# Kernel tuning notes

Hardware: AMD Instinct MI355X
Metric: run time of the kernel (lower is better)

The kernel has to match this reference:

```python
import jax, jax.numpy as jnp
import numpy as np

B, T, TREF, NBINS, H = 4096, 8192, 8192, 50, 32  # np.linspace(lo,hi,50) -> 49 bins
EPS = 1e-10


def setup_inputs() -> dict:
    key = jax.random.key(0)
    k0, k1, k2, k3, k4, k5 = jax.random.split(key, 6)
    return {
        "current_returns": jax.random.normal(k0, (B, T), jnp.float32) * 0.02,
        "reference_returns": jax.random.normal(k1, (TREF,), jnp.float32) * 0.02,
        "w1": jax.random.normal(k2, (H, 1), jnp.float32) * 0.5,   # Linear(1, H).weight
        "b1": jax.random.normal(k3, (H,), jnp.float32) * 0.1,
        "w2": jax.random.normal(k4, (H, H), jnp.float32) * 0.1,   # Linear(H, H).weight
        "b2": jax.random.normal(k5, (H,), jnp.float32) * 0.1,
    }


def _kl_from_hists(ref, curr, ref_min, ref_max):
    # Faithful to InformationTheory.kl_divergence with n_bins=50 (49 equal-width bins).
    nb = NBINS - 1
    lo = jnp.minimum(ref_min, curr.min())
    hi = jnp.maximum(ref_max, curr.max())
    width = (hi - lo) / nb

    def hist_density(x):
        # np.histogram(x, bins=linspace(lo,hi,50), density=True); all x in [lo,hi],
        # right edge goes to last bin (handled by clip).
        idx = jnp.clip(jnp.floor((x - lo) / width).astype(jnp.int32), 0, nb - 1)
        counts = jnp.zeros(nb, jnp.float32).at[idx].add(1.0)
        return counts / (x.shape[0] * width)

    p = hist_density(ref) + EPS
    q = hist_density(curr) + EPS
    p = p / p.sum()
    q = q / q.sum()
    return jnp.sum(p * jnp.log(p / q))


def reference(current_returns, reference_returns, w1, b1, w2, b2):
    ref = reference_returns
    ref_min, ref_max = ref.min(), ref.max()
    kl = jax.vmap(lambda c: _kl_from_hists(ref, c, ref_min, ref_max))(current_returns)  # [B]
    kl = jax.lax.stop_gradient(kl)  # original detaches before building kl_tensor
    x = kl[:, None]                                  # [B, 1]
    h = jax.nn.relu(x @ w1.T + b1)                   # [B, H]
    encoded = h @ w2.T + b2                          # [B, H]
    return kl, encoded
```

## Files before the change

kernel.cpp:

```cpp
#include <hip/hip_runtime.h>
#include <math.h>

constexpr int T_LEN  = 8192;
constexpr int B_ROWS = 4096;
constexpr int NB     = 49;
constexpr int NC     = 32;
constexpr int HDIM   = 32;
constexpr int FBINS  = 8192;
constexpr int RPB    = 8;
constexpr int RECW   = 52;
constexpr float EPSF = 1e-10f;

constexpr int WS_CDF_OFF    = 8;
constexpr int WS_BINNED_OFF = 8208;

#define HP(i) ((i) + ((i) >> 5))

__device__ __forceinline__ void sync_lds() {
    asm volatile("s_waitcnt lgkmcnt(0)" ::: "memory");
    __builtin_amdgcn_s_barrier();
    __builtin_amdgcn_sched_barrier(0);
}

__global__ __launch_bounds__(256)
void ref_cdf_kernel(const float* __restrict__ ref, float* __restrict__ wsf) {
    __shared__ float sv[FBINS];
    __shared__ int   hist[HP(FBINS)];
    __shared__ int   wsum[4];
    __shared__ float rmn4[4], rmx4[4];
    const int tid  = threadIdx.x;
    const int lane = tid & 63;
    const int wave = tid >> 6;

    const float4* r4 = (const float4*)ref;
    float4* sv4 = (float4*)sv;
    float mn = 3.0e38f, mx = -3.0e38f;
    #pragma unroll
    for (int i = 0; i < 8; ++i) {
        float4 v = r4[tid + i * 256];
        sv4[tid + i * 256] = v;
        mn = fminf(mn, fminf(fminf(v.x, v.y), fminf(v.z, v.w)));
        mx = fmaxf(mx, fmaxf(fmaxf(v.x, v.y), fmaxf(v.z, v.w)));
    }
    for (int i = tid; i < HP(FBINS); i += 256) hist[i] = 0;
    #pragma unroll
    for (int off = 32; off > 0; off >>= 1) {
        mn = fminf(mn, __shfl_xor(mn, off));
        mx = fmaxf(mx, __shfl_xor(mx, off));
    }
    if (lane == 0) { rmn4[wave] = mn; rmx4[wave] = mx; }
    __syncthreads();
    const float rmin = fminf(fminf(rmn4[0], rmn4[1]), fminf(rmn4[2], rmn4[3]));
    const float rmax = fmaxf(fmaxf(rmx4[0], rmx4[1]), fmaxf(rmx4[2], rmx4[3]));
    const float finv = (float)FBINS / (rmax - rmin);

    for (int i = tid; i < FBINS; i += 256) {
        int fb = min(max((int)((sv[i] - rmin) * finv), 0), FBINS - 1);
        atomicAdd(&hist[HP(fb)], 1);
    }
    __syncthreads();

    const int base = tid * 32;
    int s = 0;
    #pragma unroll
    for (int j = 0; j < 32; ++j) {
        int h = hist[HP(base + j)]; hist[HP(base + j)] = s; s += h;
    }
    const int own = s;
    int incl = s;
    #pragma unroll
    for (int off = 1; off < 64; off <<= 1) {
        int t = __shfl_up(incl, off);
        if (lane >= off) incl += t;
    }
    if (lane == 63) wsum[wave] = incl;
    __syncthreads();
    int woff = 0;
    #pragma unroll
    for (int w = 0; w < 4; ++w) if (w < wave) woff += wsum[w];
    const int add = woff + incl - own;
    #pragma unroll
    for (int j = 0; j < 32; ++j) hist[HP(base + j)] += add;
    __syncthreads();

    int* cdf = (int*)(wsf + WS_CDF_OFF);
    for (int i = tid; i < FBINS; i += 256) cdf[i] = hist[HP(i)];
    if (tid == 0) { cdf[FBINS] = T_LEN; wsf[0] = rmin; wsf[1] = rmax; }
    __syncthreads();

    float* binned = wsf + WS_BINNED_OFF;
    for (int i = tid; i < FBINS; i += 256) {
        float x = sv[i];
        int fb = min(max((int)((x - rmin) * finv), 0), FBINS - 1);
        int pos = atomicAdd(&hist[HP(fb)], 1);
        binned[pos] = x;
    }
}

__global__ __launch_bounds__(256, 2)
void kl_pipe_kernel(const float* __restrict__ cur,
                    const float* __restrict__ wsf,
                    const float* __restrict__ w1,
                    const float* __restrict__ b1,
                    const float* __restrict__ w2,
                    const float* __restrict__ b2,
                    float* __restrict__ kl_out,
                    float* __restrict__ enc_out) {
    __shared__ float    buf[2][T_LEN];
    __shared__ unsigned hq[NC * NB];
    __shared__ float    scmn[4], scmx[4];
    __shared__ float    rec[RPB][RECW];

    const int tid  = threadIdx.x;
    const int lane = tid & 63;
    const int wave = tid >> 6;
    const int rbase = blockIdx.x * RPB;
    const float* src = cur + (size_t)rbase * T_LEN;
    const float rmin = wsf[0], rmax = wsf[1];

    auto stage = [&](int r, int pbuf) {
        const float* g = src + (size_t)r * T_LEN + wave * 2048;
        #pragma unroll
        for (int i = 0; i < 8; ++i) {
            __builtin_amdgcn_global_load_lds(
                (const __attribute__((address_space(1))) void*)(g + i * 256 + lane * 4),
                (__attribute__((address_space(3))) void*)&buf[pbuf][wave * 2048 + i * 256],
                16, 0, 0);
        }
    };

    stage(0, 0);

    #pragma unroll
    for (int r = 0; r < RPB; ++r) {
        if (r + 1 < RPB) stage(r + 1, (r + 1) & 1);

        for (int i = tid; i < NC * NB; i += 256) hq[i] = 0u;

        if (r + 1 < RPB) {
            asm volatile("s_waitcnt vmcnt(8)" ::: "memory");
        } else {
            asm volatile("s_waitcnt vmcnt(0)" ::: "memory");
        }
        __builtin_amdgcn_sched_barrier(0);

        const float4* b4 = (const float4*)buf[r & 1];
        float4 v[8];
        #pragma unroll
        for (int i = 0; i < 8; ++i) v[i] = b4[wave * 512 + i * 64 + lane];

        float mn = 3.0e38f, mx = -3.0e38f;
        #pragma unroll
        for (int i = 0; i < 8; ++i) {
            mn = fminf(mn, fminf(fminf(v[i].x, v[i].y), fminf(v[i].z, v[i].w)));
            mx = fmaxf(mx, fmaxf(fmaxf(v[i].x, v[i].y), fmaxf(v[i].z, v[i].w)));
        }
        #pragma unroll
        for (int off = 32; off > 0; off >>= 1) {
            mn = fminf(mn, __shfl_xor(mn, off));
            mx = fmaxf(mx, __shfl_xor(mx, off));
        }
        if (lane == 0) { scmn[wave] = mn; scmx[wave] = mx; }
        sync_lds();

        const float lo = fminf(rmin,
            fminf(fminf(scmn[0], scmn[1]), fminf(scmn[2], scmn[3])));
        const float hi = fmaxf(rmax,
            fmaxf(fmaxf(scmx[0], scmx[1]), fmaxf(scmx[2], scmx[3])));
        const float width = (hi - lo) / (float)NB;
        const float winv = 1.0f / width, nlw = -lo * winv;

        unsigned* myq = hq + (tid & (NC - 1)) * NB;
        #pragma unroll
        for (int i = 0; i < 8; ++i) {
            int i0 = min((int)fmaf(v[i].x, winv, nlw), NB - 1);
            int i1 = min((int)fmaf(v[i].y, winv, nlw), NB - 1);
            int i2 = min((int)fmaf(v[i].z, winv, nlw), NB - 1);
            int i3 = min((int)fmaf(v[i].w, winv, nlw), NB - 1);
            atomicAdd(&myq[i0], 1u); atomicAdd(&myq[i1], 1u);
            atomicAdd(&myq[i2], 1u); atomicAdd(&myq[i3], 1u);
        }
        sync_lds();

        if (tid < NB) {
            unsigned sq = 0u;
            #pragma unroll
            for (int c = 0; c < NC; ++c) sq += hq[c * NB + tid];
            rec[r][tid] = (float)sq;
        }
        if (tid == NB)     rec[r][NB]     = lo;
        if (tid == NB + 1) rec[r][NB + 1] = width;
        sync_lds();
    }

    for (int rr = wave; rr < RPB; rr += 4) {
        const float lo = rec[rr][NB], width = rec[rr][NB + 1];
        const bool act = lane < NB;
        const float inv = 1.0f / ((float)T_LEN * width);
        float p = 0.0f, q = 0.0f;
        if (act) q = rec[rr][lane] * inv + EPSF;

        int C = T_LEN;
        if (lane < NB - 1) {
            const float kp1  = (float)(lane + 1);
            const float finv = (float)FBINS / (rmax - rmin);
            const int* cdf = (const int*)(wsf + WS_CDF_OFF);
            const float* binned = wsf + WS_BINNED_OFF;
            const float t = fmaf(width, kp1, lo);
            int fb = (int)floorf((t - rmin) * finv);
            int a  = min(max(fb - 2, 0), FBINS);
            int bb = min(max(fb + 3, 0), FBINS);
            int ia = cdf[a], ib = cdf[bb];
            C = ia;
            for (int i = ia; i < ib; i += 4) {
                float x0 = binned[i];
                float x1 = (i + 1 < ib) ? binned[i + 1] : 3.0e38f;
                float x2 = (i + 2 < ib) ? binned[i + 2] : 3.0e38f;
                float x3 = (i + 3 < ib) ? binned[i + 3] : 3.0e38f;
                C += ((x0 - lo) / width < kp1) ? 1 : 0;
                C += ((x1 - lo) / width < kp1) ? 1 : 0;
                C += ((x2 - lo) / width < kp1) ? 1 : 0;
                C += ((x3 - lo) / width < kp1) ? 1 : 0;
            }
        }
        int Cprev = __shfl_up(C, 1);
        if (lane == 0) Cprev = 0;
        if (act) p = (float)(C - Cprev) * inv + EPSF;

        float P = p, Q = q;
        #pragma unroll
        for (int off = 32; off > 0; off >>= 1) {
            P += __shfl_xor(P, off);
            Q += __shfl_xor(Q, off);
        }
        float term = 0.0f;
        if (act) {
            const float pn = p / P;
            const float qn = q / Q;
            term = pn * logf(pn / qn);
        }
        #pragma unroll
        for (int off = 32; off > 0; off >>= 1) term += __shfl_xor(term, off);
        if (lane == 0) kl_out[rbase + rr] = term;

        if (lane < HDIM) {
            float acc = b2[lane];
            #pragma unroll
            for (int t2 = 0; t2 < HDIM; ++t2) {
                float h = fmaxf(fmaf(term, w1[t2], b1[t2]), 0.0f);
                acc = fmaf(h, w2[lane * HDIM + t2], acc);
            }
            enc_out[(size_t)(rbase + rr) * HDIM + lane] = acc;
        }
    }
}

extern "C" void kernel_launch(void* const* d_in, const int* in_sizes, int n_in,
                              void* d_out, int out_size, void* d_ws, size_t ws_size,
                              hipStream_t stream) {
    const float* cur = (const float*)d_in[0];
    const float* ref = (const float*)d_in[1];
    const float* w1  = (const float*)d_in[2];
    const float* b1  = (const float*)d_in[3];
    const float* w2  = (const float*)d_in[4];
    const float* b2  = (const float*)d_in[5];
    float* out = (float*)d_out;
    float* wsf = (float*)d_ws;

    ref_cdf_kernel<<<1, 256, 0, stream>>>(ref, wsf);
    kl_pipe_kernel<<<B_ROWS / RPB, 256, 0, stream>>>(
        cur, wsf, w1, b1, w2, b2, out, out + B_ROWS);
}
```

Baseline: 49.98 us.

## Deepen row prefetch into a chunked LDS ring two rows ahead

Replaces the double-buffered whole-row staging with an 8-slot ring of 2048-float chunks, and keeps two rows of asynchronous global-to-LDS loads in flight. Min/max scanning now waits per chunk with graded vmcnt values, so compute can start before the whole row has arrived. Loads for row r+2 are issued inside the histogram loop of row r, right after each chunk slot has been read back into registers, which overlaps memory traffic with the LDS atomics. Values are read from LDS twice (once for min/max, once for binning) instead of being held in registers, and correctness depends on the vmcnt counts matching exactly.

```diff
diff --git a/kernel.cpp b/kernel.cpp
--- a/kernel.cpp
+++ b/kernel.cpp
@@ -8,6 +8,7 @@
 constexpr int HDIM   = 32;
 constexpr int FBINS  = 8192;
 constexpr int RPB    = 8;
+constexpr int CHUNK  = 2048;
 constexpr int RECW   = 52;
 constexpr float EPSF = 1e-10f;
 
@@ -15,6 +16,9 @@
 constexpr int WS_BINNED_OFF = 8208;
 
 #define HP(i) ((i) + ((i) >> 5))
+
+#define WAITV(N) do { asm volatile("s_waitcnt vmcnt(" #N ")" ::: "memory"); \
+                      __builtin_amdgcn_sched_barrier(0); } while (0)
 
 __device__ __forceinline__ void sync_lds() {
     asm volatile("s_waitcnt lgkmcnt(0)" ::: "memory");
@@ -98,7 +102,7 @@
 }
 
 __global__ __launch_bounds__(256, 2)
-void kl_pipe_kernel(const float* __restrict__ cur,
+void kl_deep_kernel(const float* __restrict__ cur,
                     const float* __restrict__ wsf,
                     const float* __restrict__ w1,
                     const float* __restrict__ b1,
@@ -106,7 +110,7 @@
                     const float* __restrict__ b2,
                     float* __restrict__ kl_out,
                     float* __restrict__ enc_out) {
-    __shared__ float    buf[2][T_LEN];
+    __shared__ float    ring[8][CHUNK];
     __shared__ unsigned hq[NC * NB];
     __shared__ float    scmn[4], scmx[4];
     __shared__ float    rec[RPB][RECW];
@@ -118,43 +122,26 @@
     const float* src = cur + (size_t)rbase * T_LEN;
     const float rmin = wsf[0], rmax = wsf[1];
 
-    auto stage = [&](int r, int pbuf) {
-        const float* g = src + (size_t)r * T_LEN + wave * 2048;
-        #pragma unroll
-        for (int i = 0; i < 8; ++i) {
+    auto issue_chunk = [&](int r, int c) {
+        const int slot = ((r & 1) << 2) | c;
+        const float* g = src + (size_t)r * T_LEN + c * CHUNK + wave * 512 + lane * 4;
+        #pragma unroll
+        for (int i = 0; i < 2; ++i) {
             __builtin_amdgcn_global_load_lds(
-                (const __attribute__((address_space(1))) void*)(g + i * 256 + lane * 4),
-                (__attribute__((address_space(3))) void*)&buf[pbuf][wave * 2048 + i * 256],
+                (const __attribute__((address_space(1))) void*)(g + i * 256),
+                (__attribute__((address_space(3))) void*)&ring[slot][wave * 512 + i * 256],
                 16, 0, 0);
         }
     };
-
-    stage(0, 0);
-
-    #pragma unroll
-    for (int r = 0; r < RPB; ++r) {
-        if (r + 1 < RPB) stage(r + 1, (r + 1) & 1);
-
-        for (int i = tid; i < NC * NB; i += 256) hq[i] = 0u;
-
-        if (r + 1 < RPB) {
-            asm volatile("s_waitcnt vmcnt(8)" ::: "memory");
-        } else {
-            asm volatile("s_waitcnt vmcnt(0)" ::: "memory");
-        }
-        __builtin_amdgcn_sched_barrier(0);
-
-        const float4* b4 = (const float4*)buf[r & 1];
-        float4 v[8];
-        #pragma unroll
-        for (int i = 0; i < 8; ++i) v[i] = b4[wave * 512 + i * 64 + lane];
-
-        float mn = 3.0e38f, mx = -3.0e38f;
-        #pragma unroll
-        for (int i = 0; i < 8; ++i) {
-            mn = fminf(mn, fminf(fminf(v[i].x, v[i].y), fminf(v[i].z, v[i].w)));
-            mx = fmaxf(mx, fmaxf(fmaxf(v[i].x, v[i].y), fmaxf(v[i].z, v[i].w)));
-        }
+    auto mmchunk = [&](int slot, float& mn, float& mx) {
+        const float4* q = (const float4*)&ring[slot][wave * 512];
+        float4 a0 = q[lane], a1 = q[lane + 64];
+        mn = fminf(mn, fminf(fminf(a0.x, a0.y), fminf(a0.z, a0.w)));
+        mx = fmaxf(mx, fmaxf(fmaxf(a0.x, a0.y), fmaxf(a0.z, a0.w)));
+        mn = fminf(mn, fminf(fminf(a1.x, a1.y), fminf(a1.z, a1.w)));
+        mx = fmaxf(mx, fmaxf(fmaxf(a1.x, a1.y), fmaxf(a1.z, a1.w)));
+    };
+    auto finrow = [&](int r, float mn, float mx) {
         #pragma unroll
         for (int off = 32; off > 0; off >>= 1) {
             mn = fminf(mn, __shfl_xor(mn, off));
@@ -162,7 +149,6 @@
         }
         if (lane == 0) { scmn[wave] = mn; scmx[wave] = mx; }
         sync_lds();
-
         const float lo = fminf(rmin,
             fminf(fminf(scmn[0], scmn[1]), fminf(scmn[2], scmn[3])));
         const float hi = fmaxf(rmax,
@@ -171,17 +157,26 @@
         const float winv = 1.0f / width, nlw = -lo * winv;
 
         unsigned* myq = hq + (tid & (NC - 1)) * NB;
-        #pragma unroll
-        for (int i = 0; i < 8; ++i) {
-            int i0 = min((int)fmaf(v[i].x, winv, nlw), NB - 1);
-            int i1 = min((int)fmaf(v[i].y, winv, nlw), NB - 1);
-            int i2 = min((int)fmaf(v[i].z, winv, nlw), NB - 1);
-            int i3 = min((int)fmaf(v[i].w, winv, nlw), NB - 1);
+        const int s0 = (r & 1) << 2;
+        #pragma unroll
+        for (int c = 0; c < 4; ++c) {
+            const float4* q = (const float4*)&ring[s0 + c][wave * 512];
+            float4 a0 = q[lane], a1 = q[lane + 64];
+            int i0 = min((int)fmaf(a0.x, winv, nlw), NB - 1);
+            int i1 = min((int)fmaf(a0.y, winv, nlw), NB - 1);
+            int i2 = min((int)fmaf(a0.z, winv, nlw), NB - 1);
+            int i3 = min((int)fmaf(a0.w, winv, nlw), NB - 1);
+            int i4 = min((int)fmaf(a1.x, winv, nlw), NB - 1);
+            int i5 = min((int)fmaf(a1.y, winv, nlw), NB - 1);
+            int i6 = min((int)fmaf(a1.z, winv, nlw), NB - 1);
+            int i7 = min((int)fmaf(a1.w, winv, nlw), NB - 1);
             atomicAdd(&myq[i0], 1u); atomicAdd(&myq[i1], 1u);
             atomicAdd(&myq[i2], 1u); atomicAdd(&myq[i3], 1u);
+            if (r + 2 < RPB) issue_chunk(r + 2, c);
+            atomicAdd(&myq[i4], 1u); atomicAdd(&myq[i5], 1u);
+            atomicAdd(&myq[i6], 1u); atomicAdd(&myq[i7], 1u);
         }
         sync_lds();
-
         if (tid < NB) {
             unsigned sq = 0u;
             #pragma unroll
@@ -191,6 +186,30 @@
         if (tid == NB)     rec[r][NB]     = lo;
         if (tid == NB + 1) rec[r][NB + 1] = width;
         sync_lds();
+        for (int i = tid; i < NC * NB; i += 256) hq[i] = 0u;
+    };
+
+    #pragma unroll
+    for (int rc = 0; rc < 8; ++rc) issue_chunk(rc >> 2, rc & 3);
+    for (int i = tid; i < NC * NB; i += 256) hq[i] = 0u;
+
+    for (int r = 0; r < RPB - 1; ++r) {
+        const int s0 = (r & 1) << 2;
+        float mn = 3.0e38f, mx = -3.0e38f;
+        WAITV(14); mmchunk(s0 + 0, mn, mx);
+        WAITV(12); mmchunk(s0 + 1, mn, mx);
+        WAITV(10); mmchunk(s0 + 2, mn, mx);
+        WAITV(8);  mmchunk(s0 + 3, mn, mx);
+        finrow(r, mn, mx);
+    }
+    {
+        const int s0 = (7 & 1) << 2;
+        float mn = 3.0e38f, mx = -3.0e38f;
+        WAITV(6); mmchunk(s0 + 0, mn, mx);
+        WAITV(4); mmchunk(s0 + 1, mn, mx);
+        WAITV(2); mmchunk(s0 + 2, mn, mx);
+        WAITV(0); mmchunk(s0 + 3, mn, mx);
+        finrow(7, mn, mx);
     }
 
     for (int rr = wave; rr < RPB; rr += 4) {
@@ -268,6 +287,6 @@
     float* wsf = (float*)d_ws;
 
     ref_cdf_kernel<<<1, 256, 0, stream>>>(ref, wsf);
-    kl_pipe_kernel<<<B_ROWS / RPB, 256, 0, stream>>>(
+    kl_deep_kernel<<<B_ROWS / RPB, 256, 0, stream>>>(
         cur, wsf, w1, b1, w2, b2, out, out + B_ROWS);
 }
```

Result: slower. 54.09 us (+8.2%).
